# Kernel tuning notes

Hardware: AMD Instinct MI355X
Metric: run time of the kernel (lower is better)

## Reference

```python
import jax, jax.numpy as jnp
import numpy as np

NUM_CLASSES = 512
CTX_TYPES = 4
FEAT_DIM = 1024
BATCH = 64
THRESH = 0.5       # context_similarity_threshold
SCALING = 5.0      # scaling_factor
SMOOTH = 0.01      # smoothing_factor


def setup_inputs() -> dict:
    key = jax.random.key(0)
    k1, k2, k3, k4 = jax.random.split(key, 4)
    x = jax.random.normal(k1, (BATCH, NUM_CLASSES, FEAT_DIM), dtype=jnp.float32)
    co_occurrence = jax.random.uniform(k2, (NUM_CLASSES, NUM_CLASSES), dtype=jnp.float32)
    class_counts = jax.random.uniform(k3, (NUM_CLASSES,), dtype=jnp.float32)
    context_embeddings = jax.random.normal(k4, (NUM_CLASSES, CTX_TYPES), dtype=jnp.float32)
    return {"x": x, "co_occurrence": co_occurrence, "class_counts": class_counts,
            "context_embeddings": context_embeddings}


def _build_edge_weights(co, counts, emb):
    C = co.shape[0]
    eye = jnp.eye(C, dtype=co.dtype)
    offdiag = 1.0 - eye
    avg_count = jnp.mean(counts)

    # normalized co-occurrence: (co_ij + s) / sqrt((n_i + s)(n_j + s)), off-diagonal only
    denom = jnp.sqrt((counts[:, None] + SMOOTH) * (counts[None, :] + SMOOTH))
    norm_co = (co + SMOOTH) / denom

    # context affinity: cosine sim * sigmoid(10 * (sim - thr))
    nemb = emb / jnp.linalg.norm(emb, axis=1, keepdims=True)
    sim = nemb @ nemb.T
    affinity = sim * jax.nn.sigmoid((sim - THRESH) * 10.0)

    # class-balance correction
    minc = jnp.minimum(counts[:, None], counts[None, :])
    maxc = jnp.maximum(counts[:, None], counts[None, :])
    balance = jnp.where((minc > SMOOTH) & (maxc > SMOOTH),
                        jnp.log1p(maxc / avg_count) * (minc / maxc),
                        SMOOTH)

    # confidence: 2 / (1 + exp(-co / scale)) - 1
    confidence = 2.0 / (1.0 + jnp.exp(-co / SCALING)) - 1.0

    ew = norm_co * affinity * balance * confidence * offdiag  # zero diagonal as in loops
    ew = jax.nn.softmax(ew * 5.0, axis=1)
    ew = ew * 0.9 + eye * 0.1
    return ew


def reference(x, co_occurrence, class_counts, context_embeddings):
    ew = _build_edge_weights(co_occurrence, class_counts, context_embeddings)
    # bmm with broadcast edge weights: [C,C] @ [B,C,D] -> [B,C,D]
    x_t = jnp.einsum('ij,bjd->bid', ew, x)
    inv_sqrt_d = 1.0 / float(np.sqrt(x.shape[-1]))
    gate = jax.nn.sigmoid(jnp.sum(x * x_t, axis=-1, keepdims=True) * inv_sqrt_d)
    return x * (1.0 - gate) + x_t * gate
```

## Files before the change

### kernel.cpp

```cpp
#include <hip/hip_runtime.h>
#include <hip/hip_bf16.h>
#include <stdint.h>

#define NC 512
#define FD 1024
#define NB 64
#define SMOOTH_ 0.01f
#define STQ 40

typedef __bf16 bf16x8 __attribute__((ext_vector_type(8)));
typedef float f32x4 __attribute__((ext_vector_type(4)));

__device__ __forceinline__ unsigned short f2bf(float f) {
    __hip_bfloat16 h = __float2bfloat16(f);
    return __builtin_bit_cast(unsigned short, h);
}
__device__ __forceinline__ float bf2f(unsigned short u) {
    unsigned int v = (unsigned int)u << 16;
    return __builtin_bit_cast(float, v);
}

__global__ __launch_bounds__(256) void build_ew(
    const float* __restrict__ co, const float* __restrict__ counts,
    const float* __restrict__ emb, unsigned short* __restrict__ ew) {
    __shared__ float s_counts[NC];
    __shared__ float s_nemb[NC * 4];
    __shared__ float s_redA[4], s_redM[4], s_redS[4];
    const int i = blockIdx.x;
    const int t = threadIdx.x;
    const int lane = t & 63, wv = t >> 6;

    float c0 = counts[t], c1 = counts[t + 256];
    s_counts[t] = c0;
    s_counts[t + 256] = c1;
    for (int r = t; r < NC; r += 256) {
        float e0 = emb[r * 4 + 0], e1 = emb[r * 4 + 1];
        float e2 = emb[r * 4 + 2], e3 = emb[r * 4 + 3];
        float inv = 1.0f / sqrtf(e0 * e0 + e1 * e1 + e2 * e2 + e3 * e3);
        s_nemb[r * 4 + 0] = e0 * inv;
        s_nemb[r * 4 + 1] = e1 * inv;
        s_nemb[r * 4 + 2] = e2 * inv;
        s_nemb[r * 4 + 3] = e3 * inv;
    }
    float p = c0 + c1;
#pragma unroll
    for (int o = 32; o; o >>= 1) p += __shfl_down(p, o);
    if (lane == 0) s_redA[wv] = p;
    __syncthreads();
    const float avg = (s_redA[0] + s_redA[1] + s_redA[2] + s_redA[3]) * (1.0f / 512.0f);

    const float ci = s_counts[i];
    const float ni0 = s_nemb[i * 4 + 0], ni1 = s_nemb[i * 4 + 1];
    const float ni2 = s_nemb[i * 4 + 2], ni3 = s_nemb[i * 4 + 3];

    float v[2];
#pragma unroll
    for (int u = 0; u < 2; ++u) {
        const int j = t + u * 256;
        const float c = co[i * NC + j];
        const float cj = s_counts[j];
        const float nco = (c + SMOOTH_) / sqrtf((ci + SMOOTH_) * (cj + SMOOTH_));
        const float sim = ni0 * s_nemb[j * 4 + 0] + ni1 * s_nemb[j * 4 + 1] +
                          ni2 * s_nemb[j * 4 + 2] + ni3 * s_nemb[j * 4 + 3];
        const float aff = sim / (1.0f + expf(-(sim - 0.5f) * 10.0f));
        const float mn = fminf(ci, cj), mx = fmaxf(ci, cj);
        const float bal = (mn > SMOOTH_ && mx > SMOOTH_)
                              ? log1pf(mx / avg) * (mn / mx)
                              : SMOOTH_;
        const float conf = 2.0f / (1.0f + expf(-c * 0.2f)) - 1.0f;
        const float e = (j == i) ? 0.0f : nco * aff * bal * conf;
        v[u] = e * 5.0f;
    }
    float m = fmaxf(v[0], v[1]);
#pragma unroll
    for (int o = 32; o; o >>= 1) m = fmaxf(m, __shfl_down(m, o));
    if (lane == 0) s_redM[wv] = m;
    __syncthreads();
    const float rowmax = fmaxf(fmaxf(s_redM[0], s_redM[1]), fmaxf(s_redM[2], s_redM[3]));
    const float e0 = expf(v[0] - rowmax), e1 = expf(v[1] - rowmax);
    float s = e0 + e1;
#pragma unroll
    for (int o = 32; o; o >>= 1) s += __shfl_down(s, o);
    if (lane == 0) s_redS[wv] = s;
    __syncthreads();
    const float scale = 0.9f / (s_redS[0] + s_redS[1] + s_redS[2] + s_redS[3]);
    const float w0 = e0 * scale + ((t == i) ? 0.1f : 0.0f);
    const float w1 = e1 * scale + ((t + 256 == i) ? 0.1f : 0.0f);
    ew[i * NC + t] = f2bf(w0);
    ew[i * NC + t + 256] = f2bf(w1);
}

__global__ __launch_bounds__(256, 3) void gemm_areg(
    const unsigned short* __restrict__ ew, const float* __restrict__ x,
    unsigned short* __restrict__ xt) {
    __shared__ __align__(16) unsigned short smT[2][128 * STQ];
    const int t = threadIdx.x;
    const int lane = t & 63, w = t >> 6;
    const int wr = w >> 1, wc = w & 1;

    const int bid = blockIdx.x;
    const int slot = bid & 7, idx = bid >> 3;
    const int bq = idx >> 5, inner = idx & 31;
    const int b = slot + bq * 8;
    const int i_t = inner >> 3, d_t = inner & 7;
    const int i0 = i_t * 128, d0 = d_t * 128;

    const int lr = lane & 15, kidx = lane >> 4;

    const unsigned short* ewp[4];
#pragma unroll
    for (int mi = 0; mi < 4; ++mi)
        ewp[mi] = ew + (size_t)(i0 + wr * 64 + mi * 16 + lr) * NC + kidx * 8;

    const int jp = t >> 4, m = t & 15;
    const float* gB0 = x + ((size_t)(b * NC) + 2 * jp) * FD + d0 + m;
    const float* gB1 = gB0 + FD;

    f32x4 acc[4][4];
#pragma unroll
    for (int mi = 0; mi < 4; ++mi)
#pragma unroll
        for (int ni = 0; ni < 4; ++ni) acc[mi][ni] = (f32x4){0.f, 0.f, 0.f, 0.f};

    bf16x8 aF[4];
    float r0[8], r1[8];

    auto LOAD_A = [&](int s) {
        const int off = s * 32;
#pragma unroll
        for (int mi = 0; mi < 4; ++mi)
            aF[mi] = *reinterpret_cast<const bf16x8*>(ewp[mi] + off);
    };
    auto LOAD_B = [&](int s) {
        const size_t off = (size_t)s * 32 * FD;
#pragma unroll
        for (int e = 0; e < 8; ++e) {
            r0[e] = gB0[off + 16 * e];
            r1[e] = gB1[off + 16 * e];
        }
    };
    auto STAGE_B = [&](int pb) {
        unsigned int* bt32 = reinterpret_cast<unsigned int*>(smT[pb]);
#pragma unroll
        for (int e = 0; e < 8; ++e) {
            const int d = m + 16 * e;
            const unsigned int val =
                (unsigned int)f2bf(r0[e]) | ((unsigned int)f2bf(r1[e]) << 16);
            bt32[d * (STQ / 2) + jp] = val;
        }
    };

    LOAD_A(0);
    LOAD_B(0);
    STAGE_B(0);
    LOAD_B(1);
    asm volatile("s_waitcnt lgkmcnt(0)" ::: "memory");
    __builtin_amdgcn_sched_barrier(0);
    __builtin_amdgcn_s_barrier();

    int p = 0;
    for (int s = 0; s < 16; ++s) {
        if (s < 15) STAGE_B(p ^ 1);
        if (s < 14) LOAD_B(s + 2);

        bf16x8 bF[4];
#pragma unroll
        for (int ni = 0; ni < 4; ++ni) {
            const int nb = wc * 64 + ni * 16 + lr;
            bF[ni] = *reinterpret_cast<const bf16x8*>(&smT[p][nb * STQ + kidx * 8]);
        }
#pragma unroll
        for (int mi = 0; mi < 4; ++mi)
#pragma unroll
            for (int ni = 0; ni < 4; ++ni)
                acc[mi][ni] = __builtin_amdgcn_mfma_f32_16x16x32_bf16(
                    aF[mi], bF[ni], acc[mi][ni], 0, 0, 0);

        if (s < 15) {
            LOAD_A(s + 1);
            asm volatile("s_waitcnt lgkmcnt(0)" ::: "memory");
            __builtin_amdgcn_sched_barrier(0);
            __builtin_amdgcn_s_barrier();
        }
        p ^= 1;
    }

    const int r0e = (lane >> 4) * 4;
#pragma unroll
    for (int mi = 0; mi < 4; ++mi)
#pragma unroll
        for (int ni = 0; ni < 4; ++ni)
#pragma unroll
            for (int r = 0; r < 4; ++r) {
                const size_t R = (size_t)(b * NC + i0 + wr * 64 + mi * 16 + r0e + r);
                xt[R * FD + d0 + wc * 64 + ni * 16 + lr] = f2bf(acc[mi][ni][r]);
            }
}

__global__ __launch_bounds__(256) void gate_out(
    const float* __restrict__ x, const unsigned short* __restrict__ xt,
    float* __restrict__ out) {
    __shared__ float s[4];
    const int row = blockIdx.x;
    const int t = threadIdx.x;
    const size_t base = (size_t)row * FD + t * 4;
    const float4 xv = *reinterpret_cast<const float4*>(x + base);
    const ushort4 uv = *reinterpret_cast<const ushort4*>(xt + base);
    const float t0 = bf2f(uv.x), t1 = bf2f(uv.y), t2 = bf2f(uv.z), t3 = bf2f(uv.w);
    float p = xv.x * t0 + xv.y * t1 + xv.z * t2 + xv.w * t3;
#pragma unroll
    for (int o = 32; o; o >>= 1) p += __shfl_down(p, o);
    if ((t & 63) == 0) s[t >> 6] = p;
    __syncthreads();
    const float dot = s[0] + s[1] + s[2] + s[3];
    const float g = 1.0f / (1.0f + expf(-dot * 0.03125f));
    float4 ov;
    ov.x = xv.x * (1.0f - g) + t0 * g;
    ov.y = xv.y * (1.0f - g) + t1 * g;
    ov.z = xv.z * (1.0f - g) + t2 * g;
    ov.w = xv.w * (1.0f - g) + t3 * g;
    *reinterpret_cast<float4*>(out + base) = ov;
}

extern "C" void kernel_launch(void* const* d_in, const int* in_sizes, int n_in,
                              void* d_out, int out_size, void* d_ws, size_t ws_size,
                              hipStream_t stream) {
    const float* x = (const float*)d_in[0];
    const float* co = (const float*)d_in[1];
    const float* counts = (const float*)d_in[2];
    const float* emb = (const float*)d_in[3];
    float* out = (float*)d_out;

    unsigned short* ew = (unsigned short*)d_ws;
    unsigned short* xt = (unsigned short*)((char*)d_ws + (1u << 20));

    build_ew<<<NC, 256, 0, stream>>>(co, counts, emb, ew);
    gemm_areg<<<2048, 256, 0, stream>>>(ew, x, xt);
    gate_out<<<NB * NC, 256, 0, stream>>>(x, xt, out);
}
```

Baseline: 147.5 us.

## Vectorize B loads/LDS stores and double-buffer A fragments in GEMM

The GEMM kernel now loads x as float2 over 8 rows per thread and packs eight bf16 values into one 16-byte LDS store, replacing scalar loads and 32-bit LDS writes. Edge-weight A fragments are double-buffered in registers and prefetched two steps ahead. The main loop is fully unrolled. The aim is fewer memory instructions and more latency hiding. In exchange, register pressure rises under the 3-blocks launch bound, and the new LDS write pattern may cause bank conflicts with stride STQ.

```diff
diff --git a/kernel.cpp b/kernel.cpp
--- a/kernel.cpp
+++ b/kernel.cpp
@@ -10,6 +10,7 @@
 
 typedef __bf16 bf16x8 __attribute__((ext_vector_type(8)));
 typedef float f32x4 __attribute__((ext_vector_type(4)));
+typedef unsigned short u16x8 __attribute__((ext_vector_type(8)));
 
 __device__ __forceinline__ unsigned short f2bf(float f) {
     __hip_bfloat16 h = __float2bfloat16(f);
@@ -90,7 +91,7 @@
     ew[i * NC + t + 256] = f2bf(w1);
 }
 
-__global__ __launch_bounds__(256, 3) void gemm_areg(
+__global__ __launch_bounds__(256, 3) void gemm_lean(
     const unsigned short* __restrict__ ew, const float* __restrict__ x,
     unsigned short* __restrict__ xt) {
     __shared__ __align__(16) unsigned short smT[2][128 * STQ];
@@ -107,14 +108,14 @@
 
     const int lr = lane & 15, kidx = lane >> 4;
 
-    const unsigned short* ewp[4];
+    const unsigned short* ewA[4];
 #pragma unroll
     for (int mi = 0; mi < 4; ++mi)
-        ewp[mi] = ew + (size_t)(i0 + wr * 64 + mi * 16 + lr) * NC + kidx * 8;
-
-    const int jp = t >> 4, m = t & 15;
-    const float* gB0 = x + ((size_t)(b * NC) + 2 * jp) * FD + d0 + m;
-    const float* gB1 = gB0 + FD;
+        ewA[mi] = ew + (size_t)(i0 + wr * 64 + mi * 16 + lr) * NC + kidx * 8;
+
+    const int jo = (t >> 4) & 3;
+    const int dp = (t >> 6) * 16 + (t & 15);
+    const float* gB = x + ((size_t)(b * NC) + 8 * jo) * FD + d0 + 2 * dp;
 
     f32x4 acc[4][4];
 #pragma unroll
@@ -122,35 +123,35 @@
 #pragma unroll
         for (int ni = 0; ni < 4; ++ni) acc[mi][ni] = (f32x4){0.f, 0.f, 0.f, 0.f};
 
-    bf16x8 aF[4];
-    float r0[8], r1[8];
-
-    auto LOAD_A = [&](int s) {
+    bf16x8 aF[2][4];
+    float2 rb[8];
+
+    auto LOAD_A = [&](int s, int buf) {
         const int off = s * 32;
 #pragma unroll
         for (int mi = 0; mi < 4; ++mi)
-            aF[mi] = *reinterpret_cast<const bf16x8*>(ewp[mi] + off);
+            aF[buf][mi] = *reinterpret_cast<const bf16x8*>(ewA[mi] + off);
     };
     auto LOAD_B = [&](int s) {
         const size_t off = (size_t)s * 32 * FD;
 #pragma unroll
-        for (int e = 0; e < 8; ++e) {
-            r0[e] = gB0[off + 16 * e];
-            r1[e] = gB1[off + 16 * e];
+        for (int r = 0; r < 8; ++r)
+            rb[r] = *reinterpret_cast<const float2*>(gB + off + (size_t)r * FD);
+    };
+    auto STAGE_B = [&](int pb) {
+#pragma unroll
+        for (int e = 0; e < 2; ++e) {
+            const int d = 2 * dp + e;
+            u16x8 pk;
+#pragma unroll
+            for (int r = 0; r < 8; ++r)
+                pk[r] = f2bf(e ? rb[r].y : rb[r].x);
+            *reinterpret_cast<u16x8*>(&smT[pb][d * STQ + 8 * jo]) = pk;
         }
     };
-    auto STAGE_B = [&](int pb) {
-        unsigned int* bt32 = reinterpret_cast<unsigned int*>(smT[pb]);
-#pragma unroll
-        for (int e = 0; e < 8; ++e) {
-            const int d = m + 16 * e;
-            const unsigned int val =
-                (unsigned int)f2bf(r0[e]) | ((unsigned int)f2bf(r1[e]) << 16);
-            bt32[d * (STQ / 2) + jp] = val;
-        }
-    };
-
-    LOAD_A(0);
+
+    LOAD_A(0, 0);
+    LOAD_A(1, 1);
     LOAD_B(0);
     STAGE_B(0);
     LOAD_B(1);
@@ -159,7 +160,9 @@
     __builtin_amdgcn_s_barrier();
 
     int p = 0;
+#pragma unroll
     for (int s = 0; s < 16; ++s) {
+        const int buf = s & 1;
         if (s < 15) STAGE_B(p ^ 1);
         if (s < 14) LOAD_B(s + 2);
 
@@ -174,10 +177,11 @@
 #pragma unroll
             for (int ni = 0; ni < 4; ++ni)
                 acc[mi][ni] = __builtin_amdgcn_mfma_f32_16x16x32_bf16(
-                    aF[mi], bF[ni], acc[mi][ni], 0, 0, 0);
+                    aF[buf][mi], bF[ni], acc[mi][ni], 0, 0, 0);
+
+        if (s + 2 < 16) LOAD_A(s + 2, buf);
 
         if (s < 15) {
-            LOAD_A(s + 1);
             asm volatile("s_waitcnt lgkmcnt(0)" ::: "memory");
             __builtin_amdgcn_sched_barrier(0);
             __builtin_amdgcn_s_barrier();
@@ -235,6 +239,6 @@
     unsigned short* xt = (unsigned short*)((char*)d_ws + (1u << 20));
 
     build_ew<<<NC, 256, 0, stream>>>(co, counts, emb, ew);
-    gemm_areg<<<2048, 256, 0, stream>>>(ew, x, xt);
+    gemm_lean<<<2048, 256, 0, stream>>>(ew, x, xt);
     gate_out<<<NB * NC, 256, 0, stream>>>(x, xt, out);
 }
```

Result: slower. 158.1 us (+7.2%).
